# Kernel tuning notes

Hardware: AMD Instinct MI355X
Metric: run time of the kernel (lower is better)

Reference implementation:

```python
import jax, jax.numpy as jnp
import numpy as np

N = 100000  # nodes
E = 1600000  # edges (avg degree 16)
F = 128  # input feature dim
D = 64   # output dim
BN_EPS = 1e-3  # keras BatchNormalization default epsilon


def setup_inputs() -> dict:
    key = jax.random.key(0)
    k1, k2, k3, k4, k5 = jax.random.split(key, 5)
    x = jax.random.normal(k1, (N, F), dtype=jnp.float32)
    kernel = jax.random.normal(k2, (F, D), dtype=jnp.float32) * (1.0 / np.sqrt(F))
    edge_vals = jax.random.uniform(k3, (E,), dtype=jnp.float32)
    rows = jax.random.randint(k4, (E,), 0, N, dtype=jnp.int32)
    cols = jax.random.randint(k5, (E,), 0, N, dtype=jnp.int32)
    return {"x": x, "kernel": kernel, "edge_vals": edge_vals,
            "rows": rows, "cols": cols, "nodes_num": N}


def reference(x, kernel, edge_vals, rows, cols, nodes_num):
    # BatchNormalization (fresh layer -> gamma=1, beta=0, batch statistics over axis 0)
    mean = jnp.mean(x, axis=0)
    var = jnp.var(x, axis=0)
    xn = (x - mean) * jax.lax.rsqrt(var + BN_EPS)
    # dense projection: [N, F] @ [F, D] -> [N, D]
    h = xn @ kernel
    # tf.sparse.softmax == per-row softmax over the nonzero adjacency values
    row_max = jax.ops.segment_max(edge_vals, rows, num_segments=nodes_num)
    e = jnp.exp(edge_vals - row_max[rows])
    row_sum = jax.ops.segment_sum(e, rows, num_segments=nodes_num)
    attn = e / row_sum[rows]  # [E]
    # sparse-dense matmul: out[i] = sum_j attn_ij * h[j]
    msgs = attn[:, None] * h[cols]  # [E, D] gather
    out = jax.ops.segment_sum(msgs, rows, num_segments=nodes_num)  # scatter-add
    return jnp.tanh(out)
```

## Files before the change

### kernel.cpp

```cpp
#include <hip/hip_runtime.h>
#include <hip/hip_fp16.h>
#include <math.h>

#define F 128
#define D 64
#define BSHIFT 9
#define CHUNK 4096
#define HCHUNK 8192
#define BCAP 16384

__global__ __launch_bounds__(256) void k_stats(const float* __restrict__ x,
                                               float* __restrict__ stats, int N) {
    int tid = threadIdx.x;
    int f = tid & 127;
    int rowOff = tid >> 7;
    float s = 0.f, sq = 0.f;
    for (int r = blockIdx.x * 2 + rowOff; r < N; r += gridDim.x * 2) {
        float v = x[(size_t)r * F + f];
        s += v; sq += v * v;
    }
    __shared__ float ls[256], lq[256];
    ls[tid] = s; lq[tid] = sq;
    __syncthreads();
    if (tid < 128) {
        atomicAdd(&stats[f],       ls[tid] + ls[tid + 128]);
        atomicAdd(&stats[128 + f], lq[tid] + lq[tid + 128]);
    }
}

__global__ __launch_bounds__(128) void k_prep(const float* __restrict__ stats,
                                              const float* __restrict__ W,
                                              float* __restrict__ Kp,
                                              float* __restrict__ bias, int N) {
    __shared__ float mean_s[F], rs_s[F];
    int t = threadIdx.x;
    float invN = 1.0f / (float)N;
    float m   = stats[t] * invN;
    float var = stats[128 + t] * invN - m * m;
    float rs  = rsqrtf(var + 1e-3f);
    mean_s[t] = m; rs_s[t] = rs;
    __syncthreads();
    for (int i = 0; i < 64; ++i) {
        int idx = t + 128 * i;
        int f = idx >> 6;
        Kp[idx] = rs_s[f] * W[idx];
    }
    if (t < D) {
        float b = 0.f;
        for (int f = 0; f < F; ++f) b -= mean_s[f] * rs_s[f] * W[f * D + t];
        bias[t] = b;
    }
}

__global__ __launch_bounds__(256) void k_gemm(const float* __restrict__ x,
                                              const float* __restrict__ Kp,
                                              const float* __restrict__ bias,
                                              __half* __restrict__ h, int N) {
    __shared__ float4 xs4[4][256];
    int tid = threadIdx.x;
    int wave = tid >> 6, lane = tid & 63;
    int base = blockIdx.x * 32 + wave * 8;
    const float4* xsrc = (const float4*)(x + (size_t)base * F);
    xs4[wave][lane]       = xsrc[lane];
    xs4[wave][lane + 64]  = xsrc[lane + 64];
    xs4[wave][lane + 128] = xsrc[lane + 128];
    xs4[wave][lane + 192] = xsrc[lane + 192];

    float bv = bias[lane];
    float acc[8];
    #pragma unroll
    for (int r = 0; r < 8; ++r) acc[r] = bv;

    const float4* xrow = xs4[wave];
    #pragma unroll 4
    for (int f4 = 0; f4 < 32; ++f4) {
        float k0 = Kp[(4 * f4 + 0) * D + lane];
        float k1 = Kp[(4 * f4 + 1) * D + lane];
        float k2 = Kp[(4 * f4 + 2) * D + lane];
        float k3 = Kp[(4 * f4 + 3) * D + lane];
        #pragma unroll
        for (int r = 0; r < 8; ++r) {
            float4 a = xrow[r * 32 + f4];
            acc[r] += a.x * k0 + a.y * k1 + a.z * k2 + a.w * k3;
        }
    }
    #pragma unroll
    for (int r = 0; r < 8; ++r)
        h[(size_t)(base + r) * D + lane] = __float2half(acc[r]);
}

__global__ __launch_bounds__(256) void k_binhist(const int* __restrict__ rows,
                                                 int* __restrict__ bincnt, int E) {
    __shared__ int lh[256];
    int tid = threadIdx.x;
    lh[tid] = 0;
    __syncthreads();
    int e0 = blockIdx.x * HCHUNK, e1 = min(E, e0 + HCHUNK);
    for (int e = e0 + tid; e < e1; e += 256)
        atomicAdd(&lh[rows[e] >> BSHIFT], 1);
    __syncthreads();
    int c = lh[tid];
    if (c > 0) atomicAdd(&bincnt[tid], c);
}

__global__ __launch_bounds__(256) void k_binscan(const int* __restrict__ bincnt,
                                                 int* __restrict__ binstart,
                                                 int* __restrict__ bincur, int E) {
    __shared__ int s0[256], s1[256];
    int t = threadIdx.x;
    int v = bincnt[t];
    s0[t] = v;
    __syncthreads();
    int* a = s0; int* b = s1;
    for (int off = 1; off < 256; off <<= 1) {
        int val = a[t] + ((t >= off) ? a[t - off] : 0);
        b[t] = val;
        __syncthreads();
        int* tmp = a; a = b; b = tmp;
    }
    int excl = a[t] - v;
    binstart[t] = excl;
    bincur[t]   = excl;
    if (t == 255) binstart[256] = E;
}

__global__ __launch_bounds__(256) void k_blocksortA(const int* __restrict__ rows,
                                                    const int* __restrict__ cols,
                                                    const float* __restrict__ ev,
                                                    int* __restrict__ bincur,
                                                    float4* __restrict__ ce_tmp, int E) {
    __shared__ int lcnt[256], lofs[256], gbase[256];
    __shared__ int sA[256], sB[256];
    __shared__ unsigned short binof[CHUNK];
    __shared__ float4 buf[CHUNK];
    int tid = threadIdx.x;
    int e0 = blockIdx.x * CHUNK, e1 = min(E, e0 + CHUNK);

    lcnt[tid] = 0;
    __syncthreads();
    for (int e = e0 + tid; e < e1; e += 256)
        atomicAdd(&lcnt[rows[e] >> BSHIFT], 1);
    __syncthreads();
    sA[tid] = lcnt[tid];
    __syncthreads();
    int* a = sA; int* b = sB;
    for (int off = 1; off < 256; off <<= 1) {
        int val = a[tid] + ((tid >= off) ? a[tid - off] : 0);
        b[tid] = val;
        __syncthreads();
        int* tmp = a; a = b; b = tmp;
    }
    lofs[tid] = a[tid] - lcnt[tid];
    __syncthreads();
    lcnt[tid] = lofs[tid];
    __syncthreads();
    for (int e = e0 + tid; e < e1; e += 256) {
        int r = rows[e];
        int bin = r >> BSHIFT;
        int slot = atomicAdd(&lcnt[bin], 1);
        buf[slot] = make_float4(__int_as_float(r), __int_as_float(cols[e]), ev[e], 0.f);
        binof[slot] = (unsigned short)bin;
    }
    __syncthreads();
    {
        int c = lcnt[tid] - lofs[tid];
        if (c > 0) gbase[tid] = atomicAdd(&bincur[tid], c);
    }
    __syncthreads();
    int n = e1 - e0;
    for (int s = tid; s < n; s += 256) {
        int bin = binof[s];
        ce_tmp[gbase[bin] + (s - lofs[bin])] = buf[s];
    }
}

__global__ __launch_bounds__(256) void k_binsortB(const float4* __restrict__ ce_tmp,
                                                  const int* __restrict__ binstart,
                                                  int* __restrict__ startm,
                                                  int* __restrict__ cnt,
                                                  float2* __restrict__ ce, int N, int E) {
    __shared__ float2 lbuf[BCAP];
    __shared__ int hist[512], ofs[512], ps[256], ps2[256];
    int tid = threadIdx.x;
    int r0 = blockIdx.x << BSHIFT;
    int gbeg = binstart[blockIdx.x];
    int gend = binstart[blockIdx.x + 1];
    int count = gend - gbeg;

    hist[tid] = 0; hist[tid + 256] = 0;
    __syncthreads();
    for (int k = tid; k < count; k += 256)
        atomicAdd(&hist[__float_as_int(ce_tmp[gbeg + k].x) - r0], 1);
    __syncthreads();
    int h0 = hist[2 * tid], h1 = hist[2 * tid + 1];
    ps[tid] = h0 + h1;
    __syncthreads();
    int* a = ps; int* b = ps2;
    for (int off = 1; off < 256; off <<= 1) {
        int val = a[tid] + ((tid >= off) ? a[tid - off] : 0);
        b[tid] = val;
        __syncthreads();
        int* tmp = a; a = b; b = tmp;
    }
    int pexcl = a[tid] - (h0 + h1);
    ofs[2 * tid]     = pexcl;
    ofs[2 * tid + 1] = pexcl + h0;
    __syncthreads();
    for (int i = tid; i < 512; i += 256) {
        int r = r0 + i;
        if (r < N) { startm[r] = gbeg + ofs[i]; cnt[r] = hist[i]; }
    }
    __syncthreads();
    hist[2 * tid]     = ofs[2 * tid];
    hist[2 * tid + 1] = ofs[2 * tid + 1];
    __syncthreads();
    if (count <= BCAP) {
        for (int k = tid; k < count; k += 256) {
            float4 t4 = ce_tmp[gbeg + k];
            int slot = atomicAdd(&hist[__float_as_int(t4.x) - r0], 1);
            lbuf[slot] = make_float2(t4.y, t4.z);
        }
        __syncthreads();
        for (int k = tid; k < count; k += 256)
            ce[gbeg + k] = lbuf[k];
    } else {
        for (int k = tid; k < count; k += 256) {
            float4 t4 = ce_tmp[gbeg + k];
            int slot = atomicAdd(&hist[__float_as_int(t4.x) - r0], 1);
            ce[gbeg + slot] = make_float2(t4.y, t4.z);
        }
    }
}

__global__ __launch_bounds__(256) void k_agg(const int* __restrict__ startm,
                                             const int* __restrict__ cnt,
                                             const float2* __restrict__ ce,
                                             const __half* __restrict__ h,
                                             float* __restrict__ out, int N) {
    int wid = threadIdx.x >> 6, lane = threadIdx.x & 63;
    int r = blockIdx.x * 4 + wid;
    if (r >= N) return;
    int base = startm[r];
    int nd   = cnt[r];
    int end  = base + nd;

    if (nd <= 64) {
        float2 e = make_float2(0.f, -INFINITY);
        if (lane < nd) e = ce[base + lane];
        float m = e.y;
        #pragma unroll
        for (int off = 32; off; off >>= 1) m = fmaxf(m, __shfl_xor(m, off));
        float w = (lane < nd) ? __expf(e.y - m) : 0.f;
        float s = w;
        #pragma unroll
        for (int off = 32; off; off >>= 1) s += __shfl_xor(s, off);
        w *= (nd > 0) ? (1.f / s) : 0.f;
        int c = __float_as_int(e.x) * D;

        float acc = 0.f;
        for (int j = 0; j < nd; j += 8) {
            int   c0 = __shfl(c, j + 0), c1 = __shfl(c, j + 1);
            int   c2 = __shfl(c, j + 2), c3 = __shfl(c, j + 3);
            int   c4 = __shfl(c, j + 4), c5 = __shfl(c, j + 5);
            int   c6 = __shfl(c, j + 6), c7 = __shfl(c, j + 7);
            float w0 = __shfl(w, j + 0), w1 = __shfl(w, j + 1);
            float w2 = __shfl(w, j + 2), w3 = __shfl(w, j + 3);
            float w4 = __shfl(w, j + 4), w5 = __shfl(w, j + 5);
            float w6 = __shfl(w, j + 6), w7 = __shfl(w, j + 7);
            acc += w0 * __half2float(h[c0 + lane]) + w1 * __half2float(h[c1 + lane])
                 + w2 * __half2float(h[c2 + lane]) + w3 * __half2float(h[c3 + lane]);
            acc += w4 * __half2float(h[c4 + lane]) + w5 * __half2float(h[c5 + lane])
                 + w6 * __half2float(h[c6 + lane]) + w7 * __half2float(h[c7 + lane]);
        }
        out[(size_t)r * D + lane] = tanhf(acc);
    } else {
        float m = -INFINITY;
        for (int i = base + lane; i < end; i += 64) m = fmaxf(m, ce[i].y);
        #pragma unroll
        for (int off = 32; off; off >>= 1) m = fmaxf(m, __shfl_xor(m, off));
        float s = 0.f;
        for (int i = base + lane; i < end; i += 64) s += __expf(ce[i].y - m);
        #pragma unroll
        for (int off = 32; off; off >>= 1) s += __shfl_xor(s, off);
        float inv = 1.f / s;
        float acc = 0.f;
        for (int i = base; i < end; ++i) {
            float2 t = ce[i];
            acc += __expf(t.y - m) * inv * __half2float(h[(size_t)__float_as_int(t.x) * D + lane]);
        }
        out[(size_t)r * D + lane] = tanhf(acc);
    }
}

__global__ __launch_bounds__(256) void k_rowmax(const float* __restrict__ ev,
                                                const int* __restrict__ rows,
                                                float* __restrict__ rmax, int E) {
    int i = blockIdx.x * 256 + threadIdx.x;
    if (i < E)
        atomicMax((unsigned int*)&rmax[rows[i]], __float_as_uint(ev[i]));
}

__global__ __launch_bounds__(256) void k_rowsum(const float* __restrict__ ev,
                                                const int* __restrict__ rows,
                                                const float* __restrict__ rmax,
                                                float* __restrict__ rsum, int E) {
    int i = blockIdx.x * 256 + threadIdx.x;
    if (i < E) {
        int r = rows[i];
        atomicAdd(&rsum[r], __expf(ev[i] - rmax[r]));
    }
}

__global__ __launch_bounds__(256) void k_scatter(const float* __restrict__ ev,
                                                 const int* __restrict__ rows,
                                                 const int* __restrict__ cols,
                                                 const float* __restrict__ rmax,
                                                 const float* __restrict__ rsum,
                                                 const __half* __restrict__ h,
                                                 float* __restrict__ out, int E) {
    int lane = threadIdx.x & 63;
    int e = blockIdx.x * 4 + (threadIdx.x >> 6);
    if (e < E) {
        int r = rows[e], c = cols[e];
        float w = __expf(ev[e] - rmax[r]) / rsum[r];
        atomicAdd(&out[(size_t)r * D + lane], w * __half2float(h[(size_t)c * D + lane]));
    }
}

__global__ __launch_bounds__(256) void k_tanh(float* __restrict__ out, int n4) {
    for (int i = blockIdx.x * 256 + threadIdx.x; i < n4; i += gridDim.x * 256) {
        float4 v = ((float4*)out)[i];
        v.x = tanhf(v.x); v.y = tanhf(v.y);
        v.z = tanhf(v.z); v.w = tanhf(v.w);
        ((float4*)out)[i] = v;
    }
}

extern "C" void kernel_launch(void* const* d_in, const int* in_sizes, int n_in,
                              void* d_out, int out_size, void* d_ws, size_t ws_size,
                              hipStream_t stream) {
    const float* x    = (const float*)d_in[0];
    const float* W    = (const float*)d_in[1];
    const float* ev   = (const float*)d_in[2];
    const int*   rows = (const int*)d_in[3];
    const int*   cols = (const int*)d_in[4];
    int N = in_sizes[0] / F;
    int E = in_sizes[2];
    float* out = (float*)d_out;
    float* ws  = (float*)d_ws;

    size_t off = 0;
    float* stats = ws + off; off += 256;
    float* Kp    = ws + off; off += F * D;
    float* bias  = ws + off; off += 64;
    off = (off + 255) & ~(size_t)255;

    int nbins = (N + (1 << BSHIFT) - 1) >> BSHIFT;
    int*   bincnt   = (int*)(ws + off);   off += 256;
    int*   binstart = (int*)(ws + off);   off += 257;
    int*   bincur   = (int*)(ws + off);   off += 256;
    off = (off + 255) & ~(size_t)255;
    int*   startm   = (int*)(ws + off);   off += N;
    int*   cnt      = (int*)(ws + off);   off += N;
    off = (off + 255) & ~(size_t)255;
    float2* ce      = (float2*)(ws + off); off += (size_t)2 * E;
    size_t hfloats  = ((size_t)N * D > (size_t)4 * E) ? (size_t)N * D : (size_t)4 * E;
    __half* h       = (__half*)(ws + off); off += hfloats;
    float4* ce_tmp  = (float4*)h;
    size_t need_csr = off * sizeof(float);

    hipMemsetAsync(stats, 0, 256 * sizeof(float), stream);
    k_stats<<<512, 256, 0, stream>>>(x, stats, N);
    k_prep <<<1, 128, 0, stream>>>(stats, W, Kp, bias, N);

    if (need_csr <= ws_size && nbins <= 256) {
        hipMemsetAsync(bincnt, 0, 256 * sizeof(int), stream);
        k_binhist<<<(E + HCHUNK - 1) / HCHUNK, 256, 0, stream>>>(rows, bincnt, E);
        k_binscan<<<1, 256, 0, stream>>>(bincnt, binstart, bincur, E);
        k_blocksortA<<<(E + CHUNK - 1) / CHUNK, 256, 0, stream>>>(rows, cols, ev, bincur, ce_tmp, E);
        k_binsortB<<<nbins, 256, 0, stream>>>(ce_tmp, binstart, startm, cnt, ce, N, E);
        k_gemm<<<N / 32, 256, 0, stream>>>(x, Kp, bias, h, N);
        k_agg <<<(N + 3) / 4, 256, 0, stream>>>(startm, cnt, ce, h, out, N);
    } else {
        size_t o2 = (256 + F * D + 64 + 255) & ~(size_t)255;
        float* rmax = ws + o2;  o2 += N;
        float* rsum = ws + o2;  o2 += N;
        __half* h2  = (__half*)(ws + o2);  o2 += (size_t)N * D / 2 + 64;
        hipMemsetAsync(rmax, 0, (size_t)2 * N * sizeof(float), stream);
        hipMemsetAsync(out, 0, (size_t)out_size * sizeof(float), stream);
        k_gemm  <<<N / 32, 256, 0, stream>>>(x, Kp, bias, h2, N);
        k_rowmax<<<(E + 255) / 256, 256, 0, stream>>>(ev, rows, rmax, E);
        k_rowsum<<<(E + 255) / 256, 256, 0, stream>>>(ev, rows, rmax, rsum, E);
        k_scatter<<<(E + 3) / 4, 256, 0, stream>>>(ev, rows, cols, rmax, rsum, h2, out, E);
        k_tanh  <<<2048, 256, 0, stream>>>(out, (N * D) / 4);
    }
}
```

Before: 323.9 us.

## Move per-row softmax into bucket-sort kernel and simplify aggregation loop

The per-row softmax normalisation now runs inside the bucket-sort kernel, on the LDS buffer or on global memory, once edges are grouped by row. The aggregation kernel then reads precomputed attention weights directly with wave-uniform loads instead of doing warp reductions and shuffles. This removes the max/sum reductions and shuffle traffic from the gather-bound aggregation. In exchange the sort kernel gains serial per-thread loops over each row's edges, which load-balance poorly on high-degree rows, and the global fallback path adds extra global reads and writes.

```diff
diff --git a/kernel.cpp b/kernel.cpp
--- a/kernel.cpp
+++ b/kernel.cpp
@@ -221,6 +221,19 @@
             lbuf[slot] = make_float2(t4.y, t4.z);
         }
         __syncthreads();
+        for (int i = tid; i < 512; i += 256) {
+            int beg = ofs[i], endd = hist[i];
+            if (endd > beg) {
+                float mx = -INFINITY;
+                for (int k = beg; k < endd; ++k) mx = fmaxf(mx, lbuf[k].y);
+                float ss = 0.f;
+                for (int k = beg; k < endd; ++k) ss += __expf(lbuf[k].y - mx);
+                float inv = 1.f / ss;
+                for (int k = beg; k < endd; ++k)
+                    lbuf[k].y = __expf(lbuf[k].y - mx) * inv;
+            }
+        }
+        __syncthreads();
         for (int k = tid; k < count; k += 256)
             ce[gbeg + k] = lbuf[k];
     } else {
@@ -229,6 +242,19 @@
             int slot = atomicAdd(&hist[__float_as_int(t4.x) - r0], 1);
             ce[gbeg + slot] = make_float2(t4.y, t4.z);
         }
+        __syncthreads();
+        for (int i = tid; i < 512; i += 256) {
+            int beg = gbeg + ofs[i], endd = gbeg + hist[i];
+            if (endd > beg) {
+                float mx = -INFINITY;
+                for (int k = beg; k < endd; ++k) mx = fmaxf(mx, ce[k].y);
+                float ss = 0.f;
+                for (int k = beg; k < endd; ++k) ss += __expf(ce[k].y - mx);
+                float inv = 1.f / ss;
+                for (int k = beg; k < endd; ++k)
+                    ce[k].y = __expf(ce[k].y - mx) * inv;
+            }
+        }
     }
 }
 
@@ -240,56 +266,33 @@
     int wid = threadIdx.x >> 6, lane = threadIdx.x & 63;
     int r = blockIdx.x * 4 + wid;
     if (r >= N) return;
-    int base = startm[r];
-    int nd   = cnt[r];
-    int end  = base + nd;
-
-    if (nd <= 64) {
-        float2 e = make_float2(0.f, -INFINITY);
-        if (lane < nd) e = ce[base + lane];
-        float m = e.y;
-        #pragma unroll
-        for (int off = 32; off; off >>= 1) m = fmaxf(m, __shfl_xor(m, off));
-        float w = (lane < nd) ? __expf(e.y - m) : 0.f;
-        float s = w;
-        #pragma unroll
-        for (int off = 32; off; off >>= 1) s += __shfl_xor(s, off);
-        w *= (nd > 0) ? (1.f / s) : 0.f;
-        int c = __float_as_int(e.x) * D;
-
-        float acc = 0.f;
-        for (int j = 0; j < nd; j += 8) {
-            int   c0 = __shfl(c, j + 0), c1 = __shfl(c, j + 1);
-            int   c2 = __shfl(c, j + 2), c3 = __shfl(c, j + 3);
-            int   c4 = __shfl(c, j + 4), c5 = __shfl(c, j + 5);
-            int   c6 = __shfl(c, j + 6), c7 = __shfl(c, j + 7);
-            float w0 = __shfl(w, j + 0), w1 = __shfl(w, j + 1);
-            float w2 = __shfl(w, j + 2), w3 = __shfl(w, j + 3);
-            float w4 = __shfl(w, j + 4), w5 = __shfl(w, j + 5);
-            float w6 = __shfl(w, j + 6), w7 = __shfl(w, j + 7);
-            acc += w0 * __half2float(h[c0 + lane]) + w1 * __half2float(h[c1 + lane])
-                 + w2 * __half2float(h[c2 + lane]) + w3 * __half2float(h[c3 + lane]);
-            acc += w4 * __half2float(h[c4 + lane]) + w5 * __half2float(h[c5 + lane])
-                 + w6 * __half2float(h[c6 + lane]) + w7 * __half2float(h[c7 + lane]);
-        }
-        out[(size_t)r * D + lane] = tanhf(acc);
-    } else {
-        float m = -INFINITY;
-        for (int i = base + lane; i < end; i += 64) m = fmaxf(m, ce[i].y);
-        #pragma unroll
-        for (int off = 32; off; off >>= 1) m = fmaxf(m, __shfl_xor(m, off));
-        float s = 0.f;
-        for (int i = base + lane; i < end; i += 64) s += __expf(ce[i].y - m);
-        #pragma unroll
-        for (int off = 32; off; off >>= 1) s += __shfl_xor(s, off);
-        float inv = 1.f / s;
-        float acc = 0.f;
-        for (int i = base; i < end; ++i) {
-            float2 t = ce[i];
-            acc += __expf(t.y - m) * inv * __half2float(h[(size_t)__float_as_int(t.x) * D + lane]);
-        }
-        out[(size_t)r * D + lane] = tanhf(acc);
-    }
+    int base = __builtin_amdgcn_readfirstlane(startm[r]);
+    int nd   = __builtin_amdgcn_readfirstlane(cnt[r]);
+    const float2* cep = ce + base;
+
+    float acc = 0.f;
+    int j = 0;
+    for (; j + 8 <= nd; j += 8) {
+        float2 t0 = cep[j + 0], t1 = cep[j + 1], t2 = cep[j + 2], t3 = cep[j + 3];
+        float2 t4 = cep[j + 4], t5 = cep[j + 5], t6 = cep[j + 6], t7 = cep[j + 7];
+        const __half* p0 = h + (size_t)__float_as_int(t0.x) * D;
+        const __half* p1 = h + (size_t)__float_as_int(t1.x) * D;
+        const __half* p2 = h + (size_t)__float_as_int(t2.x) * D;
+        const __half* p3 = h + (size_t)__float_as_int(t3.x) * D;
+        const __half* p4 = h + (size_t)__float_as_int(t4.x) * D;
+        const __half* p5 = h + (size_t)__float_as_int(t5.x) * D;
+        const __half* p6 = h + (size_t)__float_as_int(t6.x) * D;
+        const __half* p7 = h + (size_t)__float_as_int(t7.x) * D;
+        acc += t0.y * __half2float(p0[lane]) + t1.y * __half2float(p1[lane])
+             + t2.y * __half2float(p2[lane]) + t3.y * __half2float(p3[lane]);
+        acc += t4.y * __half2float(p4[lane]) + t5.y * __half2float(p5[lane])
+             + t6.y * __half2float(p6[lane]) + t7.y * __half2float(p7[lane]);
+    }
+    for (; j < nd; ++j) {
+        float2 t = cep[j];
+        acc += t.y * __half2float(h[(size_t)__float_as_int(t.x) * D + lane]);
+    }
+    out[(size_t)r * D + lane] = tanhf(acc);
 }
 
 __global__ __launch_bounds__(256) void k_rowmax(const float* __restrict__ ev,
```

Measured after the change: 325.0 us. Within noise of the previous version (+0.3%).
